# Performance work log

Hardware: AMD Instinct MI355X
Metric: run time of the kernel (lower is better)

Reference implementation:

```python
import jax, jax.numpy as jnp
import numpy as np

N, C, H, W = 16, 64, 128, 128
SHIFT = 1  # frozen value of torch module's random.randint(-2, 2) drawn at __init__


def setup_inputs() -> dict:
    key = jax.random.key(0)
    k1, k2, k3 = jax.random.split(key, 3)
    x = jax.random.normal(k1, (N, C, H, W), dtype=jnp.float32)
    # p_3: Conv2d(c, c, (1,5), padding=(0,2), bias=False) -> weight (C_out, C_in, 1, 5)
    w3 = jax.random.normal(k2, (C, C, 1, 5), dtype=jnp.float32) * (1.0 / np.sqrt(5.0 * C))
    # p_7: Conv2d(9c, c, 1, groups=c, bias=False) -> per output channel, 9 input channels: (C, 9)
    w7 = jax.random.normal(k3, (C, 9), dtype=jnp.float32) * (1.0 / 3.0)
    return {"x": x, "w3": w3, "w7": w7}


def reference(x, w3, w7):
    n, c, h, w = x.shape
    # t_1: F.unfold(x, (1,3), dilation=(1,2), padding=(0,2)) -> width offsets -2, 0, +2 (zero padded)
    xp = jnp.pad(x, ((0, 0), (0, 0), (0, 0), (2, 2)))
    t1 = jnp.stack([xp[..., 0:w], xp[..., 2:w + 2], xp[..., 4:w + 4]], axis=2)  # (n,c,3,h,w)
    # t_3: 1x5 conv, padding (0,2)
    t3 = jax.lax.conv_general_dilated(
        x, w3, window_strides=(1, 1), padding=[(0, 0), (2, 2)],
        dimension_numbers=("NCHW", "OIHW", "NCHW"))  # (n,c,h,w)
    # t_4: F.unfold(t1 as (n,3c,h,w), (3,1), padding=(1,0)) -> height offsets -1, 0, +1
    t1p = jnp.pad(t1, ((0, 0), (0, 0), (0, 0), (1, 1), (0, 0)))
    t4 = jnp.stack([t1p[..., 0:h, :], t1p[..., 1:h + 1, :], t1p[..., 2:h + 2, :]],
                   axis=3)  # (n, c, 3[w_off], 3[h_off], h, w)
    # t_5: roll along the W axis (dim 5)
    t5 = jnp.roll(t4, SHIFT, axis=5)
    # t_6: maximum of lhs (n,c,1,3,h,w) and rhs (n,c,3,3,h,w); lhs offset dim aligns with rhs dim 3
    t6 = jnp.maximum(t1[:, :, None, :, :, :], t5)  # (n,c,3,3,h,w)
    # t_7: grouped 1x1 conv, groups=c, 9 input channels per group -> 1 output channel
    t6f = t6.reshape(n, c, 9, h, w)
    t7 = jnp.einsum("nckhw,ck->nchw", t6f, w7)
    return t7 * t3
```

## Files before the change

kernel.cpp:

```cpp
#include <hip/hip_runtime.h>

#define NN 16
#define CC 64
#define HH 128
#define WW 128

#define LDS_STRIDE 72
#define T3B_STRIDE 132

typedef __attribute__((ext_vector_type(8))) short short8;
typedef __attribute__((ext_vector_type(4))) float floatx4;

__device__ __forceinline__ short f2bf(float f) {
    union { float f; unsigned u; } v; v.f = f;
    unsigned r = v.u + 0x7fffu + ((v.u >> 16) & 1u);
    return (short)(r >> 16);
}
__device__ __forceinline__ unsigned pack2bf(float lo, float hi) {
    union { float f; unsigned u; } a, b; a.f = lo; b.f = hi;
    unsigned ra = a.u + 0x7fffu + ((a.u >> 16) & 1u);
    unsigned rb = b.u + 0x7fffu + ((b.u >> 16) & 1u);
    return (ra >> 16) | (rb & 0xffff0000u);
}
__device__ __forceinline__ float bf2f(unsigned short u) {
    union { unsigned u; float f; } v; v.u = ((unsigned)u) << 16;
    return v.f;
}

__global__ __launch_bounds__(256) void prep_w(const float* __restrict__ w3,
                                              short* __restrict__ Abf) {
    int idx = blockIdx.x * 256 + threadIdx.x;
    if (idx < CC * CC * 5) {
        int tap = idx % 5;
        int ci  = (idx / 5) % CC;
        int co  = idx / (5 * CC);
        Abf[co * 320 + tap * 64 + ci] = f2bf(w3[idx]);
    }
}

__global__ __launch_bounds__(256, 4) void fused(const float* __restrict__ x,
                                                const short* __restrict__ Abf,
                                                const float* __restrict__ w7,
                                                float* __restrict__ out) {
    __shared__ __align__(16) char smem[132 * LDS_STRIDE * 2];
    short*    xsT = (short*)smem;
    unsigned* xsW = (unsigned*)smem;
    short*    t3b = (short*)smem;

    const int bid = blockIdx.x;
    const int nh  = ((bid & 7) << 8) | (bid >> 3);
    const int n   = nh >> 7;
    const int h   = nh & (HH - 1);
    const int tid = threadIdx.x;

    const float* xbase = x + (((size_t)n * CC) * HH + h) * WW;
    {
        const int cp  = tid & 31;
        const int wqg = tid >> 5;
        const float* r0 = xbase + (size_t)(2 * cp) * (HH * WW);
        const float* r1 = r0 + HH * WW;
        #pragma unroll
        for (int q = 0; q < 4; ++q) {
            int wq = wqg * 4 + q;
            float4 a = *(const float4*)(r0 + wq * 4);
            float4 b = *(const float4*)(r1 + wq * 4);
            int wp = wq * 4 + 2;
            xsW[(wp + 0) * 36 + cp] = pack2bf(a.x, b.x);
            xsW[(wp + 1) * 36 + cp] = pack2bf(a.y, b.y);
            xsW[(wp + 2) * 36 + cp] = pack2bf(a.z, b.z);
            xsW[(wp + 3) * 36 + cp] = pack2bf(a.w, b.w);
        }
        if (tid < 128) {
            int wpi = tid >> 5;
            int wpz = (wpi < 2) ? wpi : 128 + wpi;
            xsW[wpz * 36 + (tid & 31)] = 0u;
        }
    }
    __syncthreads();

    const int W    = tid >> 6;
    const int lane = tid & 63;
    const int lm   = lane & 15;
    const int g    = lane >> 4;

    floatx4 acc[8];
    #pragma unroll
    for (int nt = 0; nt < 8; ++nt) acc[nt] = (floatx4){0.f, 0.f, 0.f, 0.f};

    const short* arow = Abf + (W * 16 + lm) * 320;

    for (int ks = 0; ks < 10; ++ks) {
        const int kbase = ks * 32 + g * 8;
        const int tap   = kbase >> 6;
        const int cib   = kbase & 63;

        short8 a = *(const short8*)(arow + kbase);
        #pragma unroll
        for (int nt = 0; nt < 8; ++nt) {
            int wp = nt * 16 + lm + tap;
            short8 b = *(const short8*)&xsT[wp * LDS_STRIDE + cib];
            acc[nt] = __builtin_amdgcn_mfma_f32_16x16x32_bf16(a, b, acc[nt], 0, 0, 0);
        }
    }
    __syncthreads();

    #pragma unroll
    for (int nt = 0; nt < 8; ++nt) {
        #pragma unroll
        for (int r = 0; r < 4; ++r) {
            int co = W * 16 + g * 4 + r;
            t3b[co * T3B_STRIDE + nt * 16 + lm] = f2bf(acc[nt][r]);
        }
    }
    __syncthreads();

    float* orow = out + (((size_t)n * CC) * HH + h) * WW;
    #pragma unroll
    for (int it = 0; it < 8; ++it) {
        const int item = it * 256 + tid;
        const int flat = item * 4;
        const int w0   = flat & (WW - 1);
        const int c    = flat >> 7;
        const float* xb = x + ((size_t)(n * CC + c) * HH) * WW;

        float win[3][12];
        #pragma unroll
        for (int r = 0; r < 3; ++r) {
            int hh = h + r - 1;
            bool hok = (unsigned)hh < HH;
            #pragma unroll
            for (int q = 0; q < 3; ++q) {
                int cb = w0 - 4 + q * 4;
                float4 v = make_float4(0.f, 0.f, 0.f, 0.f);
                if (hok && (unsigned)cb < WW)
                    v = *(const float4*)(xb + hh * WW + cb);
                win[r][q * 4 + 0] = v.x; win[r][q * 4 + 1] = v.y;
                win[r][q * 4 + 2] = v.z; win[r][q * 4 + 3] = v.w;
            }
        }
        float wrap0[3] = {0.f, 0.f, 0.f}, wrap1[3] = {0.f, 0.f, 0.f};
        if (w0 == 0) {
            #pragma unroll
            for (int r = 0; r < 3; ++r) {
                int hh = h + r - 1;
                if ((unsigned)hh < HH) {
                    wrap0[r] = xb[hh * WW + 125];
                    wrap1[r] = xb[hh * WW + 127];
                }
            }
        }
        float wc[9];
        #pragma unroll
        for (int t = 0; t < 9; ++t) wc[t] = w7[c * 9 + t];

        ushort4 tv = *(const ushort4*)&t3b[c * T3B_STRIDE + w0];
        float t3v[4] = {bf2f(tv.x), bf2f(tv.y), bf2f(tv.z), bf2f(tv.w)};

        float res[4];
        #pragma unroll
        for (int e = 0; e < 4; ++e) {
            float a = 0.f;
            #pragma unroll
            for (int j = 0; j < 3; ++j) {
                #pragma unroll
                for (int i = 0; i < 3; ++i) {
                    float lhs = win[1][e + 2 * i + 2];
                    float rhs;
                    if (e == 0 && w0 == 0)
                        rhs = (j == 0) ? wrap0[i] : ((j == 1) ? wrap1[i] : 0.f);
                    else
                        rhs = win[i][e + 2 * j + 1];
                    a = fmaf(wc[j * 3 + i], fmaxf(lhs, rhs), a);
                }
            }
            res[e] = a;
        }
        float4 o;
        o.x = res[0] * t3v[0]; o.y = res[1] * t3v[1];
        o.z = res[2] * t3v[2]; o.w = res[3] * t3v[3];
        *(float4*)(orow + (size_t)c * (HH * WW) + w0) = o;
    }
}

extern "C" void kernel_launch(void* const* d_in, const int* in_sizes, int n_in,
                              void* d_out, int out_size, void* d_ws, size_t ws_size,
                              hipStream_t stream) {
    const float* x  = (const float*)d_in[0];
    const float* w3 = (const float*)d_in[1];
    const float* w7 = (const float*)d_in[2];
    float* out = (float*)d_out;

    short* Abf = (short*)d_ws;

    prep_w<<<(CC * CC * 5 + 255) / 256, 256, 0, stream>>>(w3, Abf);
    fused<<<NN * HH, 256, 0, stream>>>(x, Abf, w7, out);
}
```

Before: 154.0 us.

## Software-pipeline epilogue window loads and replace wrap loads with shuffles

The epilogue loop now precomputes per-thread pointers with branch-free zero-page redirection for out-of-bounds taps, so the boundary checks become plain loads. It prefetches the next channel's nine float4 window loads before computing the current one, and the first window load is issued before the barrier. The roll wrap-around values are taken from the lane holding w=124..127 via __shfl instead of extra global loads. This costs more registers for the double-buffered window, which may reduce occupancy under the 256x4 launch bound.

After: 146.8 us. -4.7%, faster.

```diff
diff --git a/kernel.cpp b/kernel.cpp
--- a/kernel.cpp
+++ b/kernel.cpp
@@ -28,7 +28,8 @@
 }
 
 __global__ __launch_bounds__(256) void prep_w(const float* __restrict__ w3,
-                                              short* __restrict__ Abf) {
+                                              short* __restrict__ Abf,
+                                              float* __restrict__ zp) {
     int idx = blockIdx.x * 256 + threadIdx.x;
     if (idx < CC * CC * 5) {
         int tap = idx % 5;
@@ -36,11 +37,13 @@
         int co  = idx / (5 * CC);
         Abf[co * 320 + tap * 64 + ci] = f2bf(w3[idx]);
     }
+    if (blockIdx.x == 0 && threadIdx.x < 64) zp[threadIdx.x] = 0.f;
 }
 
 __global__ __launch_bounds__(256, 4) void fused(const float* __restrict__ x,
                                                 const short* __restrict__ Abf,
                                                 const float* __restrict__ w7,
+                                                const float* __restrict__ zp,
                                                 float* __restrict__ out) {
     __shared__ __align__(16) char smem[132 * LDS_STRIDE * 2];
     short*    xsT = (short*)smem;
@@ -112,48 +115,67 @@
             t3b[co * T3B_STRIDE + nt * 16 + lm] = f2bf(acc[nt][r]);
         }
     }
+
+    const int w0  = (tid & 31) * 4;
+    const int chi = tid >> 5;
+    const bool isw = (w0 == 0);
+    const int src  = lane | 31;
+
+    const float* p[9];
+    int s[9];
+    const float* xb0 = x + (((size_t)(n * CC + chi)) * HH) * WW;
+    #pragma unroll
+    for (int r = 0; r < 3; ++r) {
+        int hh = h + r - 1;
+        bool hok = (unsigned)hh < HH;
+        #pragma unroll
+        for (int q = 0; q < 3; ++q) {
+            int cb = w0 - 4 + q * 4;
+            bool ok = hok && (unsigned)cb < WW;
+            p[r * 3 + q] = ok ? (xb0 + (size_t)hh * WW + cb) : zp;
+            s[r * 3 + q] = ok ? (8 * HH * WW) : 0;
+        }
+    }
+    const float* wcp = w7 + chi * 9;
+    int t3o = chi * T3B_STRIDE + w0;
+    float* outp = out + ((((size_t)(n * CC + chi)) * HH + h) * WW) + w0;
+
+    float4 cur[9];
+    #pragma unroll
+    for (int t = 0; t < 9; ++t) { cur[t] = *(const float4*)p[t]; p[t] += s[t]; }
+
     __syncthreads();
 
-    float* orow = out + (((size_t)n * CC) * HH + h) * WW;
     #pragma unroll
     for (int it = 0; it < 8; ++it) {
-        const int item = it * 256 + tid;
-        const int flat = item * 4;
-        const int w0   = flat & (WW - 1);
-        const int c    = flat >> 7;
-        const float* xb = x + ((size_t)(n * CC + c) * HH) * WW;
+        float4 nxt[9];
+        if (it < 7) {
+            #pragma unroll
+            for (int t = 0; t < 9; ++t) { nxt[t] = *(const float4*)p[t]; p[t] += s[t]; }
+        }
 
         float win[3][12];
         #pragma unroll
         for (int r = 0; r < 3; ++r) {
-            int hh = h + r - 1;
-            bool hok = (unsigned)hh < HH;
             #pragma unroll
             for (int q = 0; q < 3; ++q) {
-                int cb = w0 - 4 + q * 4;
-                float4 v = make_float4(0.f, 0.f, 0.f, 0.f);
-                if (hok && (unsigned)cb < WW)
-                    v = *(const float4*)(xb + hh * WW + cb);
+                float4 v = cur[r * 3 + q];
                 win[r][q * 4 + 0] = v.x; win[r][q * 4 + 1] = v.y;
                 win[r][q * 4 + 2] = v.z; win[r][q * 4 + 3] = v.w;
             }
         }
-        float wrap0[3] = {0.f, 0.f, 0.f}, wrap1[3] = {0.f, 0.f, 0.f};
-        if (w0 == 0) {
-            #pragma unroll
-            for (int r = 0; r < 3; ++r) {
-                int hh = h + r - 1;
-                if ((unsigned)hh < HH) {
-                    wrap0[r] = xb[hh * WW + 125];
-                    wrap1[r] = xb[hh * WW + 127];
-                }
-            }
-        }
+        float wrap0[3], wrap1[3];
+        #pragma unroll
+        for (int r = 0; r < 3; ++r) {
+            wrap0[r] = __shfl(win[r][5], src);
+            wrap1[r] = __shfl(win[r][7], src);
+        }
+
         float wc[9];
         #pragma unroll
-        for (int t = 0; t < 9; ++t) wc[t] = w7[c * 9 + t];
-
-        ushort4 tv = *(const ushort4*)&t3b[c * T3B_STRIDE + w0];
+        for (int t = 0; t < 9; ++t) wc[t] = wcp[t];
+
+        ushort4 tv = *(const ushort4*)&t3b[t3o];
         float t3v[4] = {bf2f(tv.x), bf2f(tv.y), bf2f(tv.z), bf2f(tv.w)};
 
         float res[4];
@@ -165,11 +187,11 @@
                 #pragma unroll
                 for (int i = 0; i < 3; ++i) {
                     float lhs = win[1][e + 2 * i + 2];
-                    float rhs;
-                    if (e == 0 && w0 == 0)
-                        rhs = (j == 0) ? wrap0[i] : ((j == 1) ? wrap1[i] : 0.f);
-                    else
-                        rhs = win[i][e + 2 * j + 1];
+                    float rhs = win[i][e + 2 * j + 1];
+                    if (e == 0)
+                        rhs = isw ? ((j == 0) ? wrap0[i]
+                                   : (j == 1) ? wrap1[i] : 0.f)
+                                  : rhs;
                     a = fmaf(wc[j * 3 + i], fmaxf(lhs, rhs), a);
                 }
             }
@@ -178,7 +200,13 @@
         float4 o;
         o.x = res[0] * t3v[0]; o.y = res[1] * t3v[1];
         o.z = res[2] * t3v[2]; o.w = res[3] * t3v[3];
-        *(float4*)(orow + (size_t)c * (HH * WW) + w0) = o;
+        *(float4*)outp = o;
+
+        wcp  += 8 * 9;
+        t3o  += 8 * T3B_STRIDE;
+        outp += (size_t)8 * HH * WW;
+        #pragma unroll
+        for (int t = 0; t < 9; ++t) cur[t] = nxt[t];
     }
 }
 
@@ -191,7 +219,8 @@
     float* out = (float*)d_out;
 
     short* Abf = (short*)d_ws;
-
-    prep_w<<<(CC * CC * 5 + 255) / 256, 256, 0, stream>>>(w3, Abf);
-    fused<<<NN * HH, 256, 0, stream>>>(x, Abf, w7, out);
-}
+    float* zp  = (float*)((char*)d_ws + 40960);
+
+    prep_w<<<(CC * CC * 5 + 255) / 256, 256, 0, stream>>>(w3, Abf, zp);
+    fused<<<NN * HH, 256, 0, stream>>>(x, Abf, w7, zp, out);
+}
```
